# Kernel tuning notes

Hardware: AMD Instinct MI355X
Metric: run time of the kernel (lower is better)

Reference implementation:

```python
import jax, jax.numpy as jnp
import numpy as np

K = 3  # == stride, neighbors per token


def setup_inputs() -> dict:
    key = jax.random.key(0)
    k1, k2, k3 = jax.random.split(key, 3)
    x = jax.random.normal(k1, (16, 64, 2048), dtype=jnp.float32)        # (B, C, T)
    W = jax.random.normal(k2, (64, 64, K), dtype=jnp.float32) * 0.05     # (O, I, K) conv1d weight
    b = jax.random.normal(k3, (64,), dtype=jnp.float32) * 0.05           # (O,) conv1d bias
    return {"x": x, "W": W, "b": b}


def reference(x, W, b):
    B, C, T = x.shape
    # pairwise squared euclidean distances over the channel dim: (B, T, T)
    nsq = jnp.sum(x * x, axis=1)                       # (B, T)
    dot = jnp.einsum('bct,bcs->bts', x, x)             # (B, T, T)
    dist = jnp.maximum(nsq[:, :, None] + nsq[:, None, :] - 2.0 * dot, 0.0)
    # K nearest neighbors (smallest distance -> top_k of negated dist)
    _, idx = jax.lax.top_k(-dist, K)                   # (B, T, K) int32 indices
    # gather neighbor features: prime[b, c, i*K + k] = x[b, c, idx[b, i, k]]
    idx_flat = idx.reshape(B, 1, T * K)
    prime = jnp.take_along_axis(x, jnp.broadcast_to(idx_flat, (B, C, T * K)), axis=2)
    # Conv1d with kernel_size=K, stride=K, padding=0 -> output length T
    out = jax.lax.conv_general_dilated(
        prime, W, window_strides=(K,), padding='VALID',
        dimension_numbers=('NCH', 'OIH', 'NCH'))
    return out + b[None, :, None]
```

## Files before the change

### kernel.cpp

```cpp
#include <hip/hip_runtime.h>

#define B_ 16
#define C_ 64
#define T_ 2048
#define O_ 64
#define KNN 3
#define HSPLIT 4
#define JCH (T_ / HSPLIT)
#define NJS (JCH / 32)

typedef short short8   __attribute__((ext_vector_type(8)));
typedef float f32x4    __attribute__((ext_vector_type(4)));
typedef unsigned short ushortx4 __attribute__((ext_vector_type(4)));

#define XT_OFF 0
#define XS_OFF (XT_OFF + B_ * T_ * C_)
#define NSQ_OFF (XS_OFF + B_ * T_ * C_)
#define WT_OFF (NSQ_OFF + B_ * T_)
#define CAND_OFF (WT_OFF + 192 * O_)

__device__ inline ushort bf16_rne(float f) {
    union { float f; unsigned u; } cv; cv.f = f;
    unsigned u = cv.u;
    u += 0x7FFF + ((u >> 16) & 1);
    return (ushort)(u >> 16);
}
__device__ inline float bf16_val(ushort h) {
    union { unsigned u; float f; } cv; cv.u = ((unsigned)h) << 16; return cv.f;
}

__global__ __launch_bounds__(256) void prep_kernel(const float* __restrict__ x,
                                                   const float* __restrict__ W,
                                                   float* __restrict__ ws) {
    float*  xT  = ws + XT_OFF;
    ushort* xs  = (ushort*)(ws + XS_OFF);
    float*  nsq = ws + NSQ_OFF;
    float*  Wt  = ws + WT_OFF;
    int blk = blockIdx.x;
    int tid = threadIdx.x;
    if (blk < B_ * (T_ / 64)) {
        int b  = (blk & 7) + 8 * ((blk >> 3) & 1);
        int t0 = (blk >> 4) * 64;
        __shared__ float tl[64 * 65];
        #pragma unroll
        for (int r = 0; r < 4; ++r) {
            int c  = r * 16 + (tid >> 4);
            int t4 = (tid & 15) * 4;
            float4 v = *(const float4*)(x + (size_t)(b * C_ + c) * T_ + t0 + t4);
            tl[c * 65 + t4 + 0] = v.x;
            tl[c * 65 + t4 + 1] = v.y;
            tl[c * 65 + t4 + 2] = v.z;
            tl[c * 65 + t4 + 3] = v.w;
        }
        __syncthreads();
        #pragma unroll
        for (int r = 0; r < 4; ++r) {
            int t  = r * 16 + (tid >> 4);
            int c0 = (tid & 15) * 4;
            float v0 = tl[(c0 + 0) * 65 + t];
            float v1 = tl[(c0 + 1) * 65 + t];
            float v2 = tl[(c0 + 2) * 65 + t];
            float v3 = tl[(c0 + 3) * 65 + t];
            size_t rowg = (size_t)(b * T_ + t0 + t);
            float4 xv; xv.x = v0; xv.y = v1; xv.z = v2; xv.w = v3;
            *(float4*)(xT + rowg * 64 + c0) = xv;
            ushort h0 = bf16_rne(v0), h1 = bf16_rne(v1);
            ushort h2 = bf16_rne(v2), h3 = bf16_rne(v3);
            ushortx4 hv; hv[0] = h0; hv[1] = h1; hv[2] = h2; hv[3] = h3;
            ushortx4 lv;
            lv[0] = bf16_rne(v0 - bf16_val(h0));
            lv[1] = bf16_rne(v1 - bf16_val(h1));
            lv[2] = bf16_rne(v2 - bf16_val(h2));
            lv[3] = bf16_rne(v3 - bf16_val(h3));
            *(ushortx4*)(xs + rowg * 128 + c0)      = hv;
            *(ushortx4*)(xs + rowg * 128 + 64 + c0) = lv;
        }
        if (tid < 64) {
            float s = 0.f;
            #pragma unroll
            for (int c = 0; c < 64; ++c) { float v = tl[c * 65 + tid]; s = fmaf(v, v, s); }
            nsq[b * T_ + t0 + tid] = s;
        }
    } else {
        int e = (blk - B_ * (T_ / 64)) * 256 + tid;
        if (e < O_ * C_ * KNN) {
            int o = e / (C_ * KNN);
            int c = (e / KNN) % C_;
            int k = e % KNN;
            Wt[(k * 64 + c) * O_ + o] = W[e];
        }
    }
}

__global__ __launch_bounds__(256, 8) void knn_mfma_kernel(const ushort* __restrict__ xs,
                                                          const float* __restrict__ nsq,
                                                          ushort* __restrict__ cand) {
    __shared__ __align__(16) ushort jbuf[2][32 * 64];
    __shared__ float nsqs[JCH];

    int bid = blockIdx.x;
    int b   = (bid & 7) + 8 * (bid >> 10);
    int h   = (bid >> 3) & 3;
    int m   = (bid >> 5) & 31;
    int i0  = m * 64;
    int tid = threadIdx.x;
    int w   = tid >> 6, l = tid & 63, lr = l & 15, lq = l >> 4;
    const ushort* xsb = xs + (size_t)b * T_ * 128;
    int jBase = h * JCH;

    if (tid < JCH / 4)
        ((float4*)nsqs)[tid] = ((const float4*)(nsq + b * T_ + jBase))[tid];

    short8 bA0, bA1;
    {
        const ushort* ia = xsb + (size_t)(i0 + w * 16 + lr) * 128 + lq * 8;
        bA0 = *(const short8*)(ia + 0);  bA1 = *(const short8*)(ia + 32);
    }
    float niA = nsq[b * T_ + i0 + w * 16 + lr] + 4.0f;

    const float INF = __builtin_inff();
    float kA0 = INF, kA1 = INF, kA2 = INF, kA3 = INF;

    int rloc_d = w * 8 + (l >> 3);
    int pc_d   = l & 7;
    int gc_d   = pc_d ^ (rloc_d & 7);
    #define ISSUE_DMA(jsv, bufv) {                                               \
        const ushort* gp = xsb + (size_t)(jBase + (jsv) * 32 + rloc_d) * 128 + gc_d * 8; \
        __builtin_amdgcn_global_load_lds(                                        \
            (const __attribute__((address_space(1))) void*)gp,                   \
            (__attribute__((address_space(3))) void*)(jbuf[bufv] + rloc_d * 64 + pc_d * 8), \
            16, 0, 0);                                                           \
    }

    asm volatile("s_waitcnt lgkmcnt(0)" ::: "memory");

    ISSUE_DMA(0, 0);

    #pragma unroll 1
    for (int js = 0; js < NJS; ++js) {
        asm volatile("s_waitcnt vmcnt(0)" ::: "memory");
        __builtin_amdgcn_s_barrier();
        asm volatile("" ::: "memory");
        __builtin_amdgcn_sched_barrier(0);
        if (js + 1 < NJS) ISSUE_DMA(js + 1, (js + 1) & 1);
        const char* jb8 = (const char*)jbuf[js & 1];
        #pragma unroll
        for (int tile = 0; tile < 2; ++tile) {
            int r = tile * 16 + lr;
            const char* rowp = jb8 + r * 128;
            short8 ah0 = *(const short8*)(rowp + (((lq)     ^ (r & 7)) << 4));
            short8 ah1 = *(const short8*)(rowp + (((4 + lq) ^ (r & 7)) << 4));
            f32x4 accA = {0.f, 0.f, 0.f, 0.f};
            accA = __builtin_amdgcn_mfma_f32_16x16x32_bf16(ah0, bA0, accA, 0, 0, 0);
            accA = __builtin_amdgcn_mfma_f32_16x16x32_bf16(ah1, bA1, accA, 0, 0, 0);
            float4 nv = *(const float4*)(nsqs + js * 32 + tile * 16 + lq * 4);
            int idb = ((js * 2 + tile) << 2) | (lq << 8);
            #define INS(K0, K1, K2, K3, sv, idv) {                                  \
                unsigned uu = (__float_as_uint(sv) & 0xFFFFFC00u) | (unsigned)(idv); \
                float kf = __uint_as_float(uu);                                      \
                float n0 = fminf(K0, kf);                                            \
                float n1 = __builtin_amdgcn_fmed3f(K0, K1, kf);                      \
                float n2 = __builtin_amdgcn_fmed3f(K1, K2, kf);                      \
                float n3 = __builtin_amdgcn_fmed3f(K2, K3, kf);                      \
                K0 = n0; K1 = n1; K2 = n2; K3 = n3; }
            {
                float s0 = fmaf(-2.f, accA[0], nv.x + niA); INS(kA0, kA1, kA2, kA3, s0, idb + 0);
                float s1 = fmaf(-2.f, accA[1], nv.y + niA); INS(kA0, kA1, kA2, kA3, s1, idb + 1);
                float s2 = fmaf(-2.f, accA[2], nv.z + niA); INS(kA0, kA1, kA2, kA3, s2, idb + 2);
                float s3 = fmaf(-2.f, accA[3], nv.w + niA); INS(kA0, kA1, kA2, kA3, s3, idb + 3);
            }
            #undef INS
        }
    }

    __syncthreads();
    float* fbuf = (float*)jbuf;
    {
        float* pa = fbuf + (w * 16 + lr) * 16 + lq * 4;
        pa[0] = kA0; pa[1] = kA1; pa[2] = kA2; pa[3] = kA3;
    }
    __syncthreads();
    if (tid < 64) {
        const float* pr = fbuf + tid * 16;
        float m0 = INF, m1 = INF, m2 = INF, m3 = INF;
        #pragma unroll
        for (int q2 = 0; q2 < 16; ++q2) {
            float kf = pr[q2];
            float n0 = fminf(m0, kf);
            float n1 = __builtin_amdgcn_fmed3f(m0, m1, kf);
            float n2 = __builtin_amdgcn_fmed3f(m1, m2, kf);
            float n3 = __builtin_amdgcn_fmed3f(m2, m3, kf);
            m0 = n0; m1 = n1; m2 = n2; m3 = n3;
        }
        ushortx4 cv;
        #define DEC(mf, slot) { unsigned u = __float_as_uint(mf) & 1023u;            \
            cv[slot] = (ushort)(jBase + (((u >> 2) & 63u) << 4) + ((u >> 8) << 2) + (u & 3)); }
        DEC(m0, 0); DEC(m1, 1); DEC(m2, 2); DEC(m3, 3);
        #undef DEC
        int row = b * T_ + i0 + tid;
        *(ushortx4*)(cand + (size_t)row * 16 + h * 4) = cv;
    }
}

__global__ __launch_bounds__(256, 4) void conv_fused_kernel(const float* __restrict__ ws,
                                                            const float* __restrict__ bias,
                                                            float* __restrict__ out) {
    const float*  xT   = ws + XT_OFF;
    const float*  nsq  = ws + NSQ_OFF;
    const float*  Wt   = ws + WT_OFF;
    const ushort* cand = (const ushort*)(ws + CAND_OFF);

    __shared__ float g_s[192 * 32];
    __shared__ int   jsel3[32 * 3];

    float* sref = g_s;
    int*   jref = (int*)(g_s + 32 * 17);
    float* q_s  = g_s + 1152;

    int bid = blockIdx.x;
    int bb  = (bid & 7) + 8 * (bid >> 9);
    int i0  = ((bid >> 3) & 63) * 32;
    int tid = threadIdx.x;
    int w = tid >> 6, l = tid & 63;
    int bT = bb * T_;

    {
        int row = tid >> 3;
        int c8  = tid & 7;
        const float4* src = (const float4*)(xT + (size_t)(bT + i0 + row) * 64 + c8 * 8);
        float4 v0 = src[0], v1 = src[1];
        *(float4*)(q_s + row * 68 + c8 * 8)     = v0;
        *(float4*)(q_s + row * 68 + c8 * 8 + 4) = v1;
    }

    const float INF = __builtin_inff();
    int cd  = l >> 2;
    int c16 = l & 3;
    int rbase = i0 + w * 8;
    int jtA[8];
    #pragma unroll
    for (int rr = 0; rr < 8; ++rr)
        jtA[rr] = cand[(size_t)(bT + rbase + rr) * 16 + cd];
    __builtin_amdgcn_sched_barrier(0);
    float nsqj[8];
    #pragma unroll
    for (int rr = 0; rr < 8; ++rr)
        nsqj[rr] = nsq[bT + jtA[rr]];

    #pragma unroll
    for (int rp = 0; rp < 2; ++rp) {
        float4 bv0[4], bv1[4], bv2[4], bv3[4];
        #pragma unroll
        for (int r4 = 0; r4 < 4; ++r4) {
            const float4* bp = (const float4*)(xT + (size_t)(bT + jtA[rp * 4 + r4]) * 64 + c16 * 16);
            bv0[r4] = bp[0]; bv1[r4] = bp[1]; bv2[r4] = bp[2]; bv3[r4] = bp[3];
        }
        __builtin_amdgcn_sched_barrier(0);
        #pragma unroll
        for (int r4 = 0; r4 < 4; ++r4) {
            int rl = w * 8 + rp * 4 + r4;
            int jt = jtA[rp * 4 + r4];
            const float4* ap = (const float4*)(q_s + rl * 68 + c16 * 16);
            float4 a0 = ap[0], a1 = ap[1], a2 = ap[2], a3 = ap[3];
            float4 b0 = bv0[r4], b1 = bv1[r4], b2 = bv2[r4], b3 = bv3[r4];
            float p0 = fmaf(b0.w, a0.w, fmaf(b0.z, a0.z, fmaf(b0.y, a0.y, b0.x * a0.x)));
            float p1 = fmaf(b1.w, a1.w, fmaf(b1.z, a1.z, fmaf(b1.y, a1.y, b1.x * a1.x)));
            float p2 = fmaf(b2.w, a2.w, fmaf(b2.z, a2.z, fmaf(b2.y, a2.y, b2.x * a2.x)));
            float p3 = fmaf(b3.w, a3.w, fmaf(b3.z, a3.z, fmaf(b3.y, a3.y, b3.x * a3.x)));
            float p = (p0 + p1) + (p2 + p3);
            p += __shfl_xor(p, 1, 64);
            p += __shfl_xor(p, 2, 64);
            float s = nsqj[rp * 4 + r4] - 2.f * p;
            if (c16 == 0) { sref[rl * 17 + cd] = s; jref[rl * 17 + cd] = jt; }
        }
    }
    __syncthreads();

    if (tid < 32) {
        const float* sp = sref + tid * 17;
        const int*   jp = jref + tid * 17;
        float D0 = INF, D1 = INF, D2 = INF;
        int   I0 = 0x7FFFFFFF, I1 = 0x7FFFFFFF, I2 = 0x7FFFFFFF;
        #pragma unroll
        for (int t = 0; t < 16; ++t) {
            float s  = sp[t];
            int   jt = jp[t];
            bool lt2 = (s < D2) || (s == D2 && jt < I2);
            bool lt1 = (s < D1) || (s == D1 && jt < I1);
            bool lt0 = (s < D0) || (s == D0 && jt < I0);
            float nD2 = lt1 ? D1 : (lt2 ? s : D2); int nI2 = lt1 ? I1 : (lt2 ? jt : I2);
            float nD1 = lt0 ? D0 : (lt1 ? s : D1); int nI1 = lt0 ? I0 : (lt1 ? jt : I1);
            D2 = nD2; I2 = nI2; D1 = nD1; I1 = nI1;
            D0 = lt0 ? s : D0; I0 = lt0 ? jt : I0;
        }
        jsel3[tid * 3 + 0] = I0; jsel3[tid * 3 + 1] = I1; jsel3[tid * 3 + 2] = I2;
    }
    __syncthreads();

    if (tid < 192) {
        int k    = tid >> 6;
        int r6   = tid & 63;
        int ip   = r6 >> 1;
        int half = r6 & 1;
        int j = jsel3[ip * 3 + k];
        const float4* src = (const float4*)(xT + (size_t)(bT + j) * 64 + half * 32);
        #pragma unroll
        for (int q = 0; q < 8; ++q) {
            float4 v = src[q];
            int mm = k * 64 + (half * 8 + q) * 4;
            g_s[(mm + 0) * 32 + ip] = v.x;
            g_s[(mm + 1) * 32 + ip] = v.y;
            g_s[(mm + 2) * 32 + ip] = v.z;
            g_s[(mm + 3) * 32 + ip] = v.w;
        }
    }
    __syncthreads();

    int oq = tid >> 4;
    int iq = tid & 15;
    float a0x = 0.f, a0y = 0.f, a1x = 0.f, a1y = 0.f;
    float a2x = 0.f, a2y = 0.f, a3x = 0.f, a3y = 0.f;
    #pragma unroll 4
    for (int mm = 0; mm < 192; ++mm) {
        float4 wv = *(const float4*)(Wt + mm * 64 + oq * 4);
        float2 gv = *(const float2*)(g_s + mm * 32 + iq * 2);
        a0x = fmaf(wv.x, gv.x, a0x); a0y = fmaf(wv.x, gv.y, a0y);
        a1x = fmaf(wv.y, gv.x, a1x); a1y = fmaf(wv.y, gv.y, a1y);
        a2x = fmaf(wv.z, gv.x, a2x); a2y = fmaf(wv.z, gv.y, a2y);
        a3x = fmaf(wv.w, gv.x, a3x); a3y = fmaf(wv.w, gv.y, a3y);
    }
    int o0 = oq * 4;
    float b0 = bias[o0], b1 = bias[o0 + 1], b2 = bias[o0 + 2], b3 = bias[o0 + 3];
    float2 r0; r0.x = a0x + b0; r0.y = a0y + b0;
    float2 r1; r1.x = a1x + b1; r1.y = a1y + b1;
    float2 r2; r2.x = a2x + b2; r2.y = a2y + b2;
    float2 r3; r3.x = a3x + b3; r3.y = a3y + b3;
    size_t ob = (size_t)(bb * O_ + o0) * T_ + i0 + iq * 2;
    *(float2*)(out + ob)          = r0;
    *(float2*)(out + ob + T_)     = r1;
    *(float2*)(out + ob + 2 * T_) = r2;
    *(float2*)(out + ob + 3 * T_) = r3;
}

extern "C" void kernel_launch(void* const* d_in, const int* in_sizes, int n_in,
                              void* d_out, int out_size, void* d_ws, size_t ws_size,
                              hipStream_t stream) {
    const float* x    = (const float*)d_in[0];
    const float* W    = (const float*)d_in[1];
    const float* bias = (const float*)d_in[2];
    float* out = (float*)d_out;
    float* ws  = (float*)d_ws;

    prep_kernel<<<B_ * (T_ / 64) + 48, 256, 0, stream>>>(x, W, ws);
    knn_mfma_kernel<<<2048, 256, 0, stream>>>(
        (const ushort*)(ws + XS_OFF), ws + NSQ_OFF, (ushort*)(ws + CAND_OFF));
    conv_fused_kernel<<<B_ * 64, 256, 0, stream>>>(ws, bias, out);
}
```

Before: 127.6 us.

## Split refine and conv into separate kernels, stage weights in LDS

Splits the fused refine+conv kernel into a refine kernel that writes the selected neighbor indices to workspace and a conv kernel that reads them back. The conv kernel copies the full 192x64 weight matrix into shared memory with async global-to-LDS loads instead of reading weights from global memory in the inner loop. This adds a kernel launch, a global round-trip for the indices and a 48KB+24KB LDS footprint, which lowers occupancy, in exchange for cheaper weight reads and separate occupancy tuning of each phase.

```diff
diff --git a/kernel.cpp b/kernel.cpp
--- a/kernel.cpp
+++ b/kernel.cpp
@@ -18,6 +18,7 @@
 #define NSQ_OFF (XS_OFF + B_ * T_ * C_)
 #define WT_OFF (NSQ_OFF + B_ * T_)
 #define CAND_OFF (WT_OFF + 192 * O_)
+#define JSEL_OFF (CAND_OFF + 262144)
 
 __device__ inline ushort bf16_rne(float f) {
     union { float f; unsigned u; } cv; cv.f = f;
@@ -133,7 +134,6 @@
     }
 
     asm volatile("s_waitcnt lgkmcnt(0)" ::: "memory");
-
     ISSUE_DMA(0, 0);
 
     #pragma unroll 1
@@ -202,20 +202,17 @@
     }
 }
 
-__global__ __launch_bounds__(256, 4) void conv_fused_kernel(const float* __restrict__ ws,
-                                                            const float* __restrict__ bias,
-                                                            float* __restrict__ out) {
+__global__ __launch_bounds__(256, 4) void refine_kernel(const float* __restrict__ ws,
+                                                        float* __restrict__ wsw) {
     const float*  xT   = ws + XT_OFF;
     const float*  nsq  = ws + NSQ_OFF;
-    const float*  Wt   = ws + WT_OFF;
     const ushort* cand = (const ushort*)(ws + CAND_OFF);
-
-    __shared__ float g_s[192 * 32];
+    int* jsel_g = (int*)(wsw + JSEL_OFF);
+
+    __shared__ float sref[32 * 17];
+    __shared__ int   jref[32 * 17];
+    __shared__ float q_s[32 * 68];
     __shared__ int   jsel3[32 * 3];
-
-    float* sref = g_s;
-    int*   jref = (int*)(g_s + 32 * 17);
-    float* q_s  = g_s + 1152;
 
     int bid = blockIdx.x;
     int bb  = (bid & 7) + 8 * (bid >> 9);
@@ -296,13 +293,40 @@
         jsel3[tid * 3 + 0] = I0; jsel3[tid * 3 + 1] = I1; jsel3[tid * 3 + 2] = I2;
     }
     __syncthreads();
+    if (tid < 96) jsel_g[(size_t)bid * 96 + tid] = jsel3[tid];
+}
+
+__global__ __launch_bounds__(256, 2) void conv_w_kernel(const float* __restrict__ ws,
+                                                        const float* __restrict__ bias,
+                                                        float* __restrict__ out) {
+    const float*  xT   = ws + XT_OFF;
+    const float*  Wt   = ws + WT_OFF;
+    const int* jsel_g  = (const int*)(ws + JSEL_OFF);
+
+    __shared__ __align__(16) float wt_s[192 * 64];
+    __shared__ float g_s[192 * 32];
+
+    int bid = blockIdx.x;
+    int bb  = (bid & 7) + 8 * (bid >> 9);
+    int i0  = ((bid >> 3) & 63) * 32;
+    int tid = threadIdx.x;
+    int bT = bb * T_;
+
+    #pragma unroll
+    for (int r = 0; r < 12; ++r) {
+        const float* gp = Wt + (r * 256 + tid) * 4;
+        __builtin_amdgcn_global_load_lds(
+            (const __attribute__((address_space(1))) void*)gp,
+            (__attribute__((address_space(3))) void*)(wt_s + (r * 256 + tid) * 4),
+            16, 0, 0);
+    }
 
     if (tid < 192) {
         int k    = tid >> 6;
         int r6   = tid & 63;
         int ip   = r6 >> 1;
         int half = r6 & 1;
-        int j = jsel3[ip * 3 + k];
+        int j = jsel_g[(size_t)bid * 96 + ip * 3 + k];
         const float4* src = (const float4*)(xT + (size_t)(bT + j) * 64 + half * 32);
         #pragma unroll
         for (int q = 0; q < 8; ++q) {
@@ -322,7 +346,7 @@
     float a2x = 0.f, a2y = 0.f, a3x = 0.f, a3y = 0.f;
     #pragma unroll 4
     for (int mm = 0; mm < 192; ++mm) {
-        float4 wv = *(const float4*)(Wt + mm * 64 + oq * 4);
+        float4 wv = *(const float4*)(wt_s + mm * 64 + oq * 4);
         float2 gv = *(const float2*)(g_s + mm * 32 + iq * 2);
         a0x = fmaf(wv.x, gv.x, a0x); a0y = fmaf(wv.x, gv.y, a0y);
         a1x = fmaf(wv.y, gv.x, a1x); a1y = fmaf(wv.y, gv.y, a1y);
@@ -354,5 +378,6 @@
     prep_kernel<<<B_ * (T_ / 64) + 48, 256, 0, stream>>>(x, W, ws);
     knn_mfma_kernel<<<2048, 256, 0, stream>>>(
         (const ushort*)(ws + XS_OFF), ws + NSQ_OFF, (ushort*)(ws + CAND_OFF));
-    conv_fused_kernel<<<B_ * 64, 256, 0, stream>>>(ws, bias, out);
-}
+    refine_kernel<<<B_ * 64, 256, 0, stream>>>(ws, ws);
+    conv_w_kernel<<<B_ * 64, 256, 0, stream>>>(ws, bias, out);
+}
```

New measurement: 124.2 us. 1.03x faster.
